# Kernel optimization log

Hardware: AMD Instinct MI355X
Metric: run time of the kernel (lower is better)

The kernel has to match this reference:

```python
import jax, jax.numpy as jnp
import numpy as np

N_NODES = 50000
N_EDGES = 800000
N_GRAPHS = 1024
BN_EPS = 1e-5

def _linear_params(key, fan_in, fan_out):
    k1, k2 = jax.random.split(key)
    lim = 1.0 / np.sqrt(fan_in)
    w = jax.random.uniform(k1, (fan_in, fan_out), jnp.float32, -lim, lim)
    b = jax.random.uniform(k2, (fan_out,), jnp.float32, -lim, lim)
    return w, b


def setup_inputs() -> dict:
    key = jax.random.key(0)
    ks = jax.random.split(key, 16)
    x = jax.random.normal(ks[0], (N_NODES, 114), jnp.float32)
    edge_index = jax.random.randint(ks[1], (2, N_EDGES), 0, N_NODES, jnp.int64)
    batch = jnp.sort(jax.random.randint(ks[2], (N_NODES,), 0, N_GRAPHS, jnp.int64))
    w1a, b1a = _linear_params(ks[3], 114, 198)
    w1b, b1b = _linear_params(ks[4], 198, 198)
    w2a, b2a = _linear_params(ks[5], 198, 64)
    w2b, b2b = _linear_params(ks[6], 64, 64)
    w3a, b3a = _linear_params(ks[7], 64, 32)
    w3b, b3b = _linear_params(ks[8], 32, 32)
    fw1, fb1 = _linear_params(ks[9], 32, 16)
    fw2, fb2 = _linear_params(ks[10], 16, 8)
    ow, ob = _linear_params(ks[11], 8, 2)
    g1 = jnp.ones((198,), jnp.float32); be1 = jnp.zeros((198,), jnp.float32)
    g2 = jnp.ones((64,), jnp.float32); be2 = jnp.zeros((64,), jnp.float32)
    g3 = jnp.ones((32,), jnp.float32); be3 = jnp.zeros((32,), jnp.float32)
    return dict(x=x, edge_index=edge_index, batch=batch,
                w1a=w1a, b1a=b1a, w1b=w1b, b1b=b1b, g1=g1, be1=be1,
                w2a=w2a, b2a=b2a, w2b=w2b, b2b=b2b, g2=g2, be2=be2,
                w3a=w3a, b3a=b3a, w3b=w3b, b3b=b3b, g3=g3, be3=be3,
                fw1=fw1, fb1=fb1, fw2=fw2, fb2=fb2, ow=ow, ob=ob)


def _gin_conv(x, src, dst, wa, ba, wb, bb):
    # GINConv, eps=0: h_i = MLP((1+eps)*x_i + sum_{j->i} x_j)
    agg = jax.ops.segment_sum(x[src], dst, num_segments=N_NODES)
    h = x + agg
    h = jax.nn.relu(h @ wa + ba) @ wb + bb
    return h


def _batchnorm(h, gamma, beta):
    # training-mode BN over the node axis (biased variance, as torch)
    mean = jnp.mean(h, axis=0)
    var = jnp.var(h, axis=0)
    return (h - mean) * jax.lax.rsqrt(var + BN_EPS) * gamma + beta


def reference(x, edge_index, batch,
              w1a, b1a, w1b, b1b, g1, be1,
              w2a, b2a, w2b, b2b, g2, be2,
              w3a, b3a, w3b, b3b, g3, be3,
              fw1, fb1, fw2, fb2, ow, ob):
    src, dst = edge_index[0], edge_index[1]
    h = jax.nn.relu(_gin_conv(x, src, dst, w1a, b1a, w1b, b1b))
    h = _batchnorm(h, g1, be1)
    h = jax.nn.relu(_gin_conv(h, src, dst, w2a, b2a, w2b, b2b))
    h = _batchnorm(h, g2, be2)
    h = jax.nn.relu(_gin_conv(h, src, dst, w3a, b3a, w3b, b3b))
    h = _batchnorm(h, g3, be3)
    g = jax.ops.segment_sum(h, batch, num_segments=N_GRAPHS)  # global_add_pool
    g = jax.nn.relu(g @ fw1 + fb1)
    g = jax.nn.relu(g @ fw2 + fb2)
    return g @ ow + ob
```

## Files before the change

### kernel.cpp

```cpp
#include <hip/hip_runtime.h>

#define NODES  50000
#define EDGES  800000
#define GRAPHS 1024
#define P      200

#define SCAN_BLK 256
#define SCAN_NB  ((NODES + SCAN_BLK - 1) / SCAN_BLK)

typedef __attribute__((ext_vector_type(8))) short short8v;
typedef __attribute__((ext_vector_type(4))) short short4v;
typedef __attribute__((ext_vector_type(4))) float f32x4;

__device__ __forceinline__ ushort f2bf(float f) {
    uint u = __float_as_uint(f);
    u = u + 0x7FFFu + ((u >> 16) & 1u);
    return (ushort)(u >> 16);
}

__global__ void hist_kernel(const int* __restrict__ dst, int* __restrict__ deg) {
    int e = blockIdx.x * blockDim.x + threadIdx.x;
    if (e < EDGES) atomicAdd(&deg[dst[e]], 1);
}

__global__ void scan_part(const int* __restrict__ deg, int* __restrict__ part) {
    __shared__ int sh[SCAN_BLK];
    int t = threadIdx.x;
    int n = blockIdx.x * SCAN_BLK + t;
    sh[t] = (n < NODES) ? deg[n] : 0;
    __syncthreads();
    for (int off = SCAN_BLK / 2; off > 0; off >>= 1) {
        if (t < off) sh[t] += sh[t + off];
        __syncthreads();
    }
    if (t == 0) part[blockIdx.x] = sh[0];
}

__global__ void scan_scan(int* __restrict__ part) {
    __shared__ int sh[SCAN_BLK];
    int t = threadIdx.x;
    int v = (t < SCAN_NB) ? part[t] : 0;
    sh[t] = v;
    __syncthreads();
    for (int off = 1; off < SCAN_BLK; off <<= 1) {
        int u = 0;
        if (t >= off) u = sh[t - off];
        __syncthreads();
        if (t >= off) sh[t] += u;
        __syncthreads();
    }
    if (t < SCAN_NB) part[t] = sh[t] - v;
}

__global__ void scan_expand(const int* __restrict__ deg, const int* __restrict__ part,
                            int* __restrict__ rowstart, int* __restrict__ cursor) {
    __shared__ int sh[SCAN_BLK];
    int t = threadIdx.x;
    int n = blockIdx.x * SCAN_BLK + t;
    int v = (n < NODES) ? deg[n] : 0;
    sh[t] = v;
    __syncthreads();
    for (int off = 1; off < SCAN_BLK; off <<= 1) {
        int u = 0;
        if (t >= off) u = sh[t - off];
        __syncthreads();
        if (t >= off) sh[t] += u;
        __syncthreads();
    }
    int excl = sh[t] - v + part[blockIdx.x];
    if (n < NODES) {
        rowstart[n] = excl;
        cursor[n]   = excl;
        if (n == NODES - 1) rowstart[NODES] = excl + v;
    }
}

__global__ void scatter_kernel(const int* __restrict__ src, const int* __restrict__ dst,
                               int* __restrict__ cursor, int* __restrict__ csrc) {
    int e = blockIdx.x * blockDim.x + threadIdx.x;
    if (e < EDGES) {
        int p = atomicAdd(&cursor[dst[e]], 1);
        csrc[p] = src[e];
    }
}

__global__ void pad_w_mfma(const float* __restrict__ W, int K, int N, int NCH, int CT,
                           ushort* __restrict__ out) {
    int s = blockIdx.x * blockDim.x + threadIdx.x;
    int half = NCH * CT * 512;
    if (s >= 2 * half) return;
    int h = s / half;
    int r = s % half;
    int j = r & 7, col = (r >> 3) & 15, kg = (r >> 7) & 3;
    int rest = r >> 9;
    int ct = rest % CT, c = rest / CT;
    int k = c * 32 + kg * 8 + j;
    int n = ct * 16 + col;
    float v = (k < K && n < N) ? W[k * N + n] : 0.0f;
    ushort hi = f2bf(v);
    if (h == 0) out[s] = hi;
    else {
        float hf = __uint_as_float(((uint)hi) << 16);
        out[s] = f2bf(v - hf);
    }
}

template<int D>
__global__ void csr_agg(const float* __restrict__ feat, int fpitch,
                        const int* __restrict__ rowstart, const int* __restrict__ csrc,
                        float* __restrict__ agg, int opitch) {
    int wid  = (blockIdx.x * blockDim.x + threadIdx.x) >> 6;
    int lane = threadIdx.x & 63;
    if (wid >= NODES) return;
    constexpr int NI  = (D + 63) / 64;
    constexpr int UNR = 8;
    float s[NI];
#pragma unroll
    for (int i = 0; i < NI; i++) s[i] = 0.0f;
    const int r0 = rowstart[wid], r1 = rowstart[wid + 1];
    for (int base = r0; base < r1; base += 64) {
        const int myidx = (base + lane < r1) ? csrc[base + lane] : 0;
        const int cnt = min(64, r1 - base);
        int t = 0;
        for (; t + UNR <= cnt; t += UNR) {
            const float* p[UNR];
#pragma unroll
            for (int u = 0; u < UNR; u++)
                p[u] = feat + (size_t)__shfl(myidx, t + u) * fpitch;
            float v[UNR][NI];
#pragma unroll
            for (int u = 0; u < UNR; u++)
#pragma unroll
                for (int i = 0; i < NI; i++) {
                    int c = lane + 64 * i;
                    if (c < D) v[u][i] = p[u][c];
                }
#pragma unroll
            for (int i = 0; i < NI; i++) {
                int c = lane + 64 * i;
                if (c < D) {
                    float acc = 0.0f;
#pragma unroll
                    for (int u = 0; u < UNR; u++) acc += v[u][i];
                    s[i] += acc;
                }
            }
        }
        for (; t < cnt; t++) {
            const float* fp2 = feat + (size_t)__shfl(myidx, t) * fpitch;
#pragma unroll
            for (int i = 0; i < NI; i++) {
                int c = lane + 64 * i;
                if (c < D) s[i] += fp2[c];
            }
        }
    }
    float* ap = agg + (size_t)wid * opitch;
#pragma unroll
    for (int i = 0; i < NI; i++) {
        int c = lane + 64 * i;
        if (c < D) ap[c] = s[i];
    }
}

template<int K, int N, bool ADD2, bool STATS, bool BNX, bool PRE, bool ACT>
__launch_bounds__(256)
__global__ void gemm_mfma(const float* __restrict__ X, int xpitch,
                          const float* __restrict__ A2, int apitch,
                          const ushort* __restrict__ WF,
                          const float* __restrict__ B,
                          const float* __restrict__ PREB,
                          const float* __restrict__ scale, const float* __restrict__ shift,
                          float* __restrict__ OUT, int opitch,
                          float* __restrict__ gsum, float* __restrict__ gsq) {
    constexpr int KP  = ((K + 31) / 32) * 32;
    constexpr int NCH = KP / 32;
    constexpr int NP  = ((N + 63) / 64) * 64;
    constexpr int CT  = NP / 16;
    constexpr int CTW = CT / 4;
    static_assert(CT % 4 == 0, "col tiles must split across 4 waves");

    __shared__ __align__(16) ushort A_lds[2][2][2][4][16][8];
    __shared__ float shSum[STATS ? NP : 4];
    __shared__ float shSq [STATS ? NP : 4];

    const int tid  = threadIdx.x;
    const int lane = tid & 63;
    const int wv   = tid >> 6;
    const int node0 = blockIdx.x * 32;

    if (STATS) {
        for (int n = tid; n < NP; n += 256) { shSum[n] = 0.0f; shSq[n] = 0.0f; }
    }

    f32x4 acc[2][CTW] = {};

    const int sr  = tid >> 3;
    const int sc4 = (tid & 7) * 4;
    const int skg = sc4 >> 3;
    const int sj0 = sc4 & 7;
    const int gn  = node0 + sr;
    const size_t fstride = (size_t)NCH * CT * 512;

    float xvA[4], xvB[4];
    float a2vA[ADD2 ? 4 : 1], a2vB[ADD2 ? 4 : 1];

    auto loadA_A = [&](int c) {
        const int k0 = c * 32 + sc4;
#pragma unroll
        for (int j = 0; j < 4; j++) {
            int gk = k0 + j;
            bool ok = (gn < NODES && gk < K);
            xvA[j] = ok ? X[(size_t)gn * xpitch + gk] : 0.0f;
            if (ADD2) a2vA[j] = ok ? A2[(size_t)gn * apitch + gk] : 0.0f;
        }
    };
    auto loadA_B = [&](int c) {
        const int k0 = c * 32 + sc4;
#pragma unroll
        for (int j = 0; j < 4; j++) {
            int gk = k0 + j;
            bool ok = (gn < NODES && gk < K);
            xvB[j] = ok ? X[(size_t)gn * xpitch + gk] : 0.0f;
            if (ADD2) a2vB[j] = ok ? A2[(size_t)gn * apitch + gk] : 0.0f;
        }
    };
    auto cvtCore = [&](int buf, int c, const float* xv, const float* a2v) {
        const int k0 = c * 32 + sc4;
        short4v hv, lv;
#pragma unroll
        for (int j = 0; j < 4; j++) {
            int gk = k0 + j;
            float t = 0.0f;
            if (gn < NODES && gk < K) {
                t = xv[j];
                if (BNX) t = fmaf(t, scale[gk], shift[gk]);
                if (ADD2) t += a2v[j];
                if (PRE)  t = fmaxf(t + PREB[gk], 0.0f);
            }
            ushort h = f2bf(t);
            float hf = __uint_as_float(((uint)h) << 16);
            ushort l = f2bf(t - hf);
            hv[j] = (short)h; lv[j] = (short)l;
        }
        *(short4v*)&A_lds[buf][0][sr >> 4][skg][sr & 15][sj0] = hv;
        *(short4v*)&A_lds[buf][1][sr >> 4][skg][sr & 15][sj0] = lv;
    };

    loadA_A(0);
    if (NCH > 1) loadA_B(1);
    cvtCore(0, 0, xvA, ADD2 ? a2vA : xvA);
    __syncthreads();

    const int kg = lane >> 4, rw = lane & 15;
#pragma unroll
    for (int c = 0; c < NCH; c++) {
        const int buf = c & 1;
        if (c + 2 < NCH) {
            if ((c & 1) == 0) loadA_A(c + 2);
            else              loadA_B(c + 2);
        }

        short8v ah[2], al[2];
#pragma unroll
        for (int rt = 0; rt < 2; rt++) {
            ah[rt] = *(const short8v*)&A_lds[buf][0][rt][kg][rw][0];
            al[rt] = *(const short8v*)&A_lds[buf][1][rt][kg][rw][0];
        }

        const size_t fb0 = ((size_t)(c * CT + wv * CTW)) * 512 + (size_t)lane * 8;
        short8v wh = *(const short8v*)(WF + fb0);
        short8v wl = *(const short8v*)(WF + fstride + fb0);
#pragma unroll
        for (int t = 0; t < CTW; t++) {
            short8v nwh, nwl;
            if (t + 1 < CTW) {
                const size_t fb = fb0 + (size_t)(t + 1) * 512;
                nwh = *(const short8v*)(WF + fb);
                nwl = *(const short8v*)(WF + fstride + fb);
            }
            __builtin_amdgcn_s_setprio(1);
#pragma unroll
            for (int rt = 0; rt < 2; rt++) {
                acc[rt][t] = __builtin_amdgcn_mfma_f32_16x16x32_bf16(ah[rt], wh, acc[rt][t], 0, 0, 0);
                acc[rt][t] = __builtin_amdgcn_mfma_f32_16x16x32_bf16(al[rt], wh, acc[rt][t], 0, 0, 0);
                acc[rt][t] = __builtin_amdgcn_mfma_f32_16x16x32_bf16(ah[rt], wl, acc[rt][t], 0, 0, 0);
            }
            __builtin_amdgcn_s_setprio(0);
            if (t + 1 < CTW) { wh = nwh; wl = nwl; }
        }

        if (c + 1 < NCH) {
            if (((c + 1) & 1) == 0) cvtCore((c + 1) & 1, c + 1, xvA, ADD2 ? a2vA : xvA);
            else                    cvtCore((c + 1) & 1, c + 1, xvB, ADD2 ? a2vB : xvB);
        }
        __syncthreads();
    }

    const int mg = lane >> 4, colb = lane & 15;
#pragma unroll
    for (int t = 0; t < CTW; t++) {
        const int ct = wv * CTW + t;
        const int n = ct * 16 + colb;
        const float bn = (ACT && n < N) ? B[n] : 0.0f;
        float psum = 0.0f, psq = 0.0f;
#pragma unroll
        for (int rt = 0; rt < 2; rt++) {
#pragma unroll
            for (int j = 0; j < 4; j++) {
                int m = node0 + rt * 16 + mg * 4 + j;
                float vv = ACT ? fmaxf(acc[rt][t][j] + bn, 0.0f) : acc[rt][t][j];
                if (m < NODES && n < N) {
                    OUT[(size_t)m * opitch + n] = vv;
                    if (STATS) { psum += vv; psq += vv * vv; }
                }
            }
        }
        if (STATS && n < N) {
            atomicAdd(&shSum[n], psum);
            atomicAdd(&shSq[n], psq);
        }
    }
    if (STATS) {
        __syncthreads();
        for (int n = tid; n < N; n += 256) {
            atomicAdd(&gsum[n], shSum[n]);
            atomicAdd(&gsq[n], shSq[n]);
        }
    }
}

template<int N>
__global__ void bn_finalize(const float* __restrict__ sum, const float* __restrict__ sq,
                            const float* __restrict__ gamma, const float* __restrict__ beta,
                            float* __restrict__ scale, float* __restrict__ shift) {
    int n = threadIdx.x;
    if (n < N) {
        float mean = sum[n] * (1.0f / NODES);
        float var  = sq[n] * (1.0f / NODES) - mean * mean;
        var = var < 0.0f ? 0.0f : var;
        float sc = gamma[n] * rsqrtf(var + 1e-5f);
        scale[n] = sc;
        shift[n] = beta[n] - mean * sc;
    }
}

__global__ void pool_kernel(const float* __restrict__ h, const int* __restrict__ batch,
                            const float* __restrict__ scale, const float* __restrict__ shift,
                            float* __restrict__ g) {
    int idx = blockIdx.x * blockDim.x + threadIdx.x;
    if (idx >= NODES * 32) return;
    int n = idx >> 5, f = idx & 31;
    float v = fmaf(h[(size_t)n * 32 + f], scale[f], shift[f]);
    atomicAdd(&g[batch[n] * 32 + f], v);
}

__global__ void head_kernel(const float* __restrict__ g,
                            const float* __restrict__ fw1, const float* __restrict__ fb1,
                            const float* __restrict__ fw2, const float* __restrict__ fb2,
                            const float* __restrict__ ow, const float* __restrict__ ob,
                            float* __restrict__ out) {
    int gi = blockIdx.x * blockDim.x + threadIdx.x;
    if (gi >= GRAPHS) return;
    float v[32];
#pragma unroll
    for (int k = 0; k < 32; k++) v[k] = g[gi * 32 + k];
    float a1[16];
#pragma unroll
    for (int o = 0; o < 16; o++) {
        float s = fb1[o];
#pragma unroll
        for (int k = 0; k < 32; k++) s = fmaf(v[k], fw1[k * 16 + o], s);
        a1[o] = s > 0.0f ? s : 0.0f;
    }
    float a2[8];
#pragma unroll
    for (int o = 0; o < 8; o++) {
        float s = fb2[o];
#pragma unroll
        for (int k = 0; k < 16; k++) s = fmaf(a1[k], fw2[k * 8 + o], s);
        a2[o] = s > 0.0f ? s : 0.0f;
    }
#pragma unroll
    for (int o = 0; o < 2; o++) {
        float s = ob[o];
#pragma unroll
        for (int k = 0; k < 8; k++) s = fmaf(a2[k], ow[k * 2 + o], s);
        out[gi * 2 + o] = s;
    }
}

extern "C" void kernel_launch(void* const* d_in, const int* in_sizes, int n_in,
                              void* d_out, int out_size, void* d_ws, size_t ws_size,
                              hipStream_t stream) {
    const float* x     = (const float*)d_in[0];
    const int*   ei    = (const int*)d_in[1];
    const int*   batch = (const int*)d_in[2];
    const float *w1a = (const float*)d_in[3],  *b1a = (const float*)d_in[4];
    const float *w1b = (const float*)d_in[5],  *b1b = (const float*)d_in[6];
    const float *g1  = (const float*)d_in[7],  *be1 = (const float*)d_in[8];
    const float *w2a = (const float*)d_in[9],  *b2a = (const float*)d_in[10];
    const float *w2b = (const float*)d_in[11], *b2b = (const float*)d_in[12];
    const float *g2  = (const float*)d_in[13], *be2 = (const float*)d_in[14];
    const float *w3a = (const float*)d_in[15], *b3a = (const float*)d_in[16];
    const float *w3b = (const float*)d_in[17], *b3b = (const float*)d_in[18];
    const float *g3  = (const float*)d_in[19], *be3 = (const float*)d_in[20];
    const float *fw1 = (const float*)d_in[21], *fb1 = (const float*)d_in[22];
    const float *fw2 = (const float*)d_in[23], *fb2 = (const float*)d_in[24];
    const float *ow  = (const float*)d_in[25], *ob  = (const float*)d_in[26];
    const int* src = ei;
    const int* dst = ei + EDGES;

    float* ws    = (float*)d_ws;
    float* b0    = ws;
    float* b1    = ws + (size_t)NODES * P;
    float* Y2    = b1;
    float* AG2   = b1 + (size_t)NODES * 64;
    float* Y3    = b1;
    float* AG3   = b1 + (size_t)NODES * 32;
    float* SUM   = ws + (size_t)2 * NODES * P;
    float* SQ    = SUM + 256;
    float* SCALE = SUM + 512;
    float* SHIFT = SUM + 768;
    float* G     = SUM + 1024;
    int*   deg      = (int*)(G + GRAPHS * 32);
    int*   rowstart = deg + NODES;
    int*   cursor   = rowstart + NODES + 1;
    int*   part     = cursor + NODES;
    int*   csrc     = part + 256;
    uintptr_t wfp = ((uintptr_t)(csrc + EDGES) + 15) & ~(uintptr_t)15;
    ushort* WF1 = (ushort*)wfp;
    ushort* WF2 = WF1 + 65536;
    ushort* WF3 = WF2 + 114688;
    ushort* WF4 = WF3 + 28672;
    ushort* WF5 = WF4 + 8192;
    ushort* WF6 = WF5 + 8192;
    float* out = (float*)d_out;

    const int GBR = (NODES + 31) / 32;
    const int AB = (NODES * 64 + 255) / 256;
    const int EB = (EDGES + 255) / 256;

    pad_w_mfma<<<(65536 + 255) / 256, 256, 0, stream>>>(w1a, 114, 198, 4, 16, WF1);
    pad_w_mfma<<<(114688 + 255) / 256, 256, 0, stream>>>(w1b, 198, 198, 7, 16, WF2);
    pad_w_mfma<<<(28672 + 255) / 256, 256, 0, stream>>>(w2a, 198, 64, 7, 4, WF3);
    pad_w_mfma<<<(8192 + 255) / 256, 256, 0, stream>>>(w2b, 64, 64, 2, 4, WF4);
    pad_w_mfma<<<(8192 + 255) / 256, 256, 0, stream>>>(w3a, 64, 32, 2, 4, WF5);
    pad_w_mfma<<<(4096 + 255) / 256, 256, 0, stream>>>(w3b, 32, 32, 1, 4, WF6);

    hipMemsetAsync(deg, 0, NODES * sizeof(int), stream);
    hist_kernel<<<EB, 256, 0, stream>>>(dst, deg);
    scan_part<<<SCAN_NB, SCAN_BLK, 0, stream>>>(deg, part);
    scan_scan<<<1, SCAN_BLK, 0, stream>>>(part);
    scan_expand<<<SCAN_NB, SCAN_BLK, 0, stream>>>(deg, part, rowstart, cursor);
    scatter_kernel<<<EB, 256, 0, stream>>>(src, dst, cursor, csrc);

    csr_agg<114><<<AB, 256, 0, stream>>>(x, 114, rowstart, csrc, b0, P);
    gemm_mfma<114, 198, true, false, false, false, true><<<GBR, 256, 0, stream>>>(
        x, 114, b0, P, WF1, b1a, nullptr, nullptr, nullptr, b1, P, nullptr, nullptr);
    hipMemsetAsync(SUM, 0, 512 * sizeof(float), stream);
    gemm_mfma<198, 198, false, true, false, false, true><<<GBR, 256, 0, stream>>>(
        b1, P, nullptr, 0, WF2, b1b, nullptr, nullptr, nullptr, b0, P, SUM, SQ);
    bn_finalize<198><<<1, 256, 0, stream>>>(SUM, SQ, g1, be1, SCALE, SHIFT);

    gemm_mfma<198, 64, false, false, true, false, false><<<GBR, 256, 0, stream>>>(
        b0, P, nullptr, 0, WF3, nullptr, nullptr, SCALE, SHIFT, Y2, 64, nullptr, nullptr);
    csr_agg<64><<<AB, 256, 0, stream>>>(Y2, 64, rowstart, csrc, AG2, 64);
    hipMemsetAsync(SUM, 0, 512 * sizeof(float), stream);
    gemm_mfma<64, 64, true, true, false, true, true><<<GBR, 256, 0, stream>>>(
        Y2, 64, AG2, 64, WF4, b2b, b2a, nullptr, nullptr, b0, 64, SUM, SQ);
    bn_finalize<64><<<1, 256, 0, stream>>>(SUM, SQ, g2, be2, SCALE, SHIFT);

    gemm_mfma<64, 32, false, false, true, false, false><<<GBR, 256, 0, stream>>>(
        b0, 64, nullptr, 0, WF5, nullptr, nullptr, SCALE, SHIFT, Y3, 32, nullptr, nullptr);
    csr_agg<32><<<AB, 256, 0, stream>>>(Y3, 32, rowstart, csrc, AG3, 32);
    hipMemsetAsync(SUM, 0, 512 * sizeof(float), stream);
    gemm_mfma<32, 32, true, true, false, true, true><<<GBR, 256, 0, stream>>>(
        Y3, 32, AG3, 32, WF6, b3b, b3a, nullptr, nullptr, b0, 32, SUM, SQ);
    bn_finalize<32><<<1, 256, 0, stream>>>(SUM, SQ, g3, be3, SCALE, SHIFT);

    hipMemsetAsync(G, 0, GRAPHS * 32 * sizeof(float), stream);
    pool_kernel<<<(NODES * 32 + 255) / 256, 256, 0, stream>>>(b0, batch, SCALE, SHIFT, G);
    head_kernel<<<(GRAPHS + 255) / 256, 256, 0, stream>>>(G, fw1, fb1, fw2, fb2, ow, ob, out);
}
```

Before: 485.2 us.

## Fuse layer-1 GIN MLP GEMMs into one kernel keeping hidden activations in LDS

Replaces the two back-to-back layer-1 MFMA GEMM launches with a single kernel. Each 32-node block computes relu(XW1a+b) and writes the hidden tile, split into bf16 hi/lo parts, into shared memory. It then runs the second GEMM from LDS and accumulates the BN statistics in the same kernel. This removes the round trip of the 50000x200 fp32 intermediate through global memory, plus one launch. The cost is larger LDS use per block, and the input and output now alias the same buffer through restrict pointers. Each block reads its own rows before it overwrites them, so the aliasing relies on that ordering.

```diff
diff --git a/kernel.cpp b/kernel.cpp
--- a/kernel.cpp
+++ b/kernel.cpp
@@ -160,6 +160,201 @@
     for (int i = 0; i < NI; i++) {
         int c = lane + 64 * i;
         if (c < D) ap[c] = s[i];
+    }
+}
+
+__launch_bounds__(256)
+__global__ void gemm_fused_l1(const float* __restrict__ X,
+                              const float* __restrict__ A2,
+                              const ushort* __restrict__ WF1,
+                              const float* __restrict__ B1,
+                              const ushort* __restrict__ WF2,
+                              const float* __restrict__ B2,
+                              float* __restrict__ OUT,
+                              float* __restrict__ gsum, float* __restrict__ gsq) {
+    constexpr int K1   = 114;
+    constexpr int NCH1 = 4;
+    constexpr int NCH2 = 7;
+    constexpr int CT   = 16;
+    constexpr int CTW  = 4;
+    constexpr int NN   = 198;
+
+    __shared__ __align__(16) ushort A_lds[2][2][2][4][16][8];
+    __shared__ __align__(16) ushort M_lds[2][NCH2][2][4][16][8];
+    __shared__ float shSum[256];
+    __shared__ float shSq [256];
+
+    const int tid  = threadIdx.x;
+    const int lane = tid & 63;
+    const int wv   = tid >> 6;
+    const int node0 = blockIdx.x * 32;
+
+    for (int n = tid; n < 256; n += 256) { shSum[n] = 0.0f; shSq[n] = 0.0f; }
+
+    const int sr  = tid >> 3;
+    const int sc4 = (tid & 7) * 4;
+    const int skg = sc4 >> 3;
+    const int sj0 = sc4 & 7;
+    const int gn  = node0 + sr;
+    const size_t fstride1 = (size_t)NCH1 * CT * 512;
+    const size_t fstride2 = (size_t)NCH2 * CT * 512;
+
+    float xv[4];
+    float a2v[4];
+
+    auto loadA = [&](int c) {
+        const int k0 = c * 32 + sc4;
+#pragma unroll
+        for (int j = 0; j < 4; j++) {
+            int gk = k0 + j;
+            bool ok = (gn < NODES && gk < K1);
+            xv[j]  = ok ? X[(size_t)gn * K1 + gk] : 0.0f;
+            a2v[j] = ok ? A2[(size_t)gn * P + gk] : 0.0f;
+        }
+    };
+    auto cvtStore = [&](int buf, int c) {
+        const int k0 = c * 32 + sc4;
+        short4v hv, lv;
+#pragma unroll
+        for (int j = 0; j < 4; j++) {
+            int gk = k0 + j;
+            float t = 0.0f;
+            if (gn < NODES && gk < K1) t = xv[j] + a2v[j];
+            ushort h = f2bf(t);
+            float hf = __uint_as_float(((uint)h) << 16);
+            ushort l = f2bf(t - hf);
+            hv[j] = (short)h; lv[j] = (short)l;
+        }
+        *(short4v*)&A_lds[buf][0][sr >> 4][skg][sr & 15][sj0] = hv;
+        *(short4v*)&A_lds[buf][1][sr >> 4][skg][sr & 15][sj0] = lv;
+    };
+
+    f32x4 acc1[2][CTW] = {};
+    loadA(0);
+    cvtStore(0, 0);
+    __syncthreads();
+
+    const int kg = lane >> 4, rw = lane & 15;
+#pragma unroll
+    for (int c = 0; c < NCH1; c++) {
+        const int buf = c & 1;
+        if (c + 1 < NCH1) loadA(c + 1);
+
+        short8v ah[2], al[2];
+#pragma unroll
+        for (int rt = 0; rt < 2; rt++) {
+            ah[rt] = *(const short8v*)&A_lds[buf][0][rt][kg][rw][0];
+            al[rt] = *(const short8v*)&A_lds[buf][1][rt][kg][rw][0];
+        }
+        const size_t fb0 = ((size_t)(c * CT + wv * CTW)) * 512 + (size_t)lane * 8;
+        short8v wh = *(const short8v*)(WF1 + fb0);
+        short8v wl = *(const short8v*)(WF1 + fstride1 + fb0);
+#pragma unroll
+        for (int t = 0; t < CTW; t++) {
+            short8v nwh, nwl;
+            if (t + 1 < CTW) {
+                const size_t fb = fb0 + (size_t)(t + 1) * 512;
+                nwh = *(const short8v*)(WF1 + fb);
+                nwl = *(const short8v*)(WF1 + fstride1 + fb);
+            }
+            __builtin_amdgcn_s_setprio(1);
+#pragma unroll
+            for (int rt = 0; rt < 2; rt++) {
+                acc1[rt][t] = __builtin_amdgcn_mfma_f32_16x16x32_bf16(ah[rt], wh, acc1[rt][t], 0, 0, 0);
+                acc1[rt][t] = __builtin_amdgcn_mfma_f32_16x16x32_bf16(al[rt], wh, acc1[rt][t], 0, 0, 0);
+                acc1[rt][t] = __builtin_amdgcn_mfma_f32_16x16x32_bf16(ah[rt], wl, acc1[rt][t], 0, 0, 0);
+            }
+            __builtin_amdgcn_s_setprio(0);
+            if (t + 1 < CTW) { wh = nwh; wl = nwl; }
+        }
+        if (c + 1 < NCH1) cvtStore((c + 1) & 1, c + 1);
+        __syncthreads();
+    }
+
+    const int mg = lane >> 4, colb = lane & 15;
+#pragma unroll
+    for (int t = 0; t < CTW; t++) {
+        const int ct = wv * CTW + t;
+        if (ct >= 14) continue;
+        const int n = ct * 16 + colb;
+        const float bn = (n < NN) ? B1[n] : 0.0f;
+        const int c2 = n >> 5, kg2 = (n >> 3) & 3, j2 = n & 7;
+#pragma unroll
+        for (int rt = 0; rt < 2; rt++) {
+#pragma unroll
+            for (int j = 0; j < 4; j++) {
+                float vv = fmaxf(acc1[rt][t][j] + bn, 0.0f);
+                if (n >= NN) vv = 0.0f;
+                ushort h = f2bf(vv);
+                float hf = __uint_as_float(((uint)h) << 16);
+                ushort l = f2bf(vv - hf);
+                int row = mg * 4 + j;
+                M_lds[0][c2][rt][kg2][row][j2] = h;
+                M_lds[1][c2][rt][kg2][row][j2] = l;
+            }
+        }
+    }
+    __syncthreads();
+
+    f32x4 acc2[2][CTW] = {};
+#pragma unroll
+    for (int c = 0; c < NCH2; c++) {
+        short8v ah[2], al[2];
+#pragma unroll
+        for (int rt = 0; rt < 2; rt++) {
+            ah[rt] = *(const short8v*)&M_lds[0][c][rt][kg][rw][0];
+            al[rt] = *(const short8v*)&M_lds[1][c][rt][kg][rw][0];
+        }
+        const size_t fb0 = ((size_t)(c * CT + wv * CTW)) * 512 + (size_t)lane * 8;
+        short8v wh = *(const short8v*)(WF2 + fb0);
+        short8v wl = *(const short8v*)(WF2 + fstride2 + fb0);
+#pragma unroll
+        for (int t = 0; t < CTW; t++) {
+            short8v nwh, nwl;
+            if (t + 1 < CTW) {
+                const size_t fb = fb0 + (size_t)(t + 1) * 512;
+                nwh = *(const short8v*)(WF2 + fb);
+                nwl = *(const short8v*)(WF2 + fstride2 + fb);
+            }
+            __builtin_amdgcn_s_setprio(1);
+#pragma unroll
+            for (int rt = 0; rt < 2; rt++) {
+                acc2[rt][t] = __builtin_amdgcn_mfma_f32_16x16x32_bf16(ah[rt], wh, acc2[rt][t], 0, 0, 0);
+                acc2[rt][t] = __builtin_amdgcn_mfma_f32_16x16x32_bf16(al[rt], wh, acc2[rt][t], 0, 0, 0);
+                acc2[rt][t] = __builtin_amdgcn_mfma_f32_16x16x32_bf16(ah[rt], wl, acc2[rt][t], 0, 0, 0);
+            }
+            __builtin_amdgcn_s_setprio(0);
+            if (t + 1 < CTW) { wh = nwh; wl = nwl; }
+        }
+    }
+
+#pragma unroll
+    for (int t = 0; t < CTW; t++) {
+        const int ct = wv * CTW + t;
+        const int n = ct * 16 + colb;
+        const float bn = (n < NN) ? B2[n] : 0.0f;
+        float psum = 0.0f, psq = 0.0f;
+#pragma unroll
+        for (int rt = 0; rt < 2; rt++) {
+#pragma unroll
+            for (int j = 0; j < 4; j++) {
+                int m = node0 + rt * 16 + mg * 4 + j;
+                float vv = fmaxf(acc2[rt][t][j] + bn, 0.0f);
+                if (m < NODES && n < NN) {
+                    OUT[(size_t)m * P + n] = vv;
+                    psum += vv; psq += vv * vv;
+                }
+            }
+        }
+        if (n < NN) {
+            atomicAdd(&shSum[n], psum);
+            atomicAdd(&shSq[n], psq);
+        }
+    }
+    __syncthreads();
+    for (int n = tid; n < NN; n += 256) {
+        atomicAdd(&gsum[n], shSum[n]);
+        atomicAdd(&gsq[n], shSq[n]);
     }
 }
 
@@ -456,11 +651,8 @@
     scatter_kernel<<<EB, 256, 0, stream>>>(src, dst, cursor, csrc);
 
     csr_agg<114><<<AB, 256, 0, stream>>>(x, 114, rowstart, csrc, b0, P);
-    gemm_mfma<114, 198, true, false, false, false, true><<<GBR, 256, 0, stream>>>(
-        x, 114, b0, P, WF1, b1a, nullptr, nullptr, nullptr, b1, P, nullptr, nullptr);
     hipMemsetAsync(SUM, 0, 512 * sizeof(float), stream);
-    gemm_mfma<198, 198, false, true, false, false, true><<<GBR, 256, 0, stream>>>(
-        b1, P, nullptr, 0, WF2, b1b, nullptr, nullptr, nullptr, b0, P, SUM, SQ);
+    gemm_fused_l1<<<GBR, 256, 0, stream>>>(x, b0, WF1, b1a, WF2, b1b, b0, SUM, SQ);
     bn_finalize<198><<<1, 256, 0, stream>>>(SUM, SQ, g1, be1, SCALE, SHIFT);
 
     gemm_mfma<198, 64, false, false, true, false, false><<<GBR, 256, 0, stream>>>(
```

After: 452.6 us. 1.07x faster.
